# Performance work log

Hardware: AMD Instinct MI355X
Metric: run time of the kernel (lower is better)

Reference implementation:

```python
import jax, jax.numpy as jnp
import numpy as np

N, E, F_IN, D, H, ED = 100000, 250000, 10, 128, 4, 5  # nodes, edges, feat_dim, hidden, heads, edge_dim

def setup_inputs() -> dict:
    key = jax.random.key(0)
    ks = jax.random.split(key, 16)
    def w(k, shape, fan_in):
        return (jax.random.normal(k, shape, jnp.float32) / np.sqrt(fan_in).astype(np.float32))
    return {
        "x": jax.random.normal(ks[0], (N, F_IN), jnp.float32),
        "edge_index": jax.random.randint(ks[1], (2, E), 0, N, dtype=jnp.int32),
        "edge_attr": jax.random.uniform(ks[2], (E, ED), jnp.float32),
        "batch": jnp.zeros((N,), jnp.int32),
        # input_proj: Linear(10,128) + BN
        "W_in": w(ks[3], (F_IN, D), F_IN), "b_in": jnp.zeros((D,), jnp.float32),
        "g_in": jnp.ones((D,), jnp.float32), "beta_in": jnp.zeros((D,), jnp.float32),
        # GINEConv: edge lin (5->128) + MLP 128->256->128 with BN
        "We": w(ks[4], (ED, D), ED), "be": jnp.zeros((D,), jnp.float32),
        "W1": w(ks[5], (D, 2 * D), D), "b1": jnp.zeros((2 * D,), jnp.float32),
        "g1": jnp.ones((2 * D,), jnp.float32), "beta1": jnp.zeros((2 * D,), jnp.float32),
        "W2": w(ks[6], (2 * D, D), 2 * D), "b2": jnp.zeros((D,), jnp.float32),
        # skip weights (pre-sigmoid) and per-layer BatchNorms
        "skip0": jnp.float32(0.5), "skip1": jnp.float32(0.5),
        "g_n0": jnp.ones((D,), jnp.float32), "b_n0": jnp.zeros((D,), jnp.float32),
        "g_n1": jnp.ones((D,), jnp.float32), "b_n1": jnp.zeros((D,), jnp.float32),
        # GATv2Conv(128,128,heads=4,concat=False,edge_dim=5)
        "Wl": w(ks[7], (D, H * D), D), "bl": jnp.zeros((H * D,), jnp.float32),
        "Wr": w(ks[8], (D, H * D), D), "br": jnp.zeros((H * D,), jnp.float32),
        "att": w(ks[9], (H, D), D),
        "W_eg": w(ks[10], (ED, H * D), ED),
        "bias_gat": jnp.zeros((D,), jnp.float32),
    }

def _bn(h, g, b):
    # BatchNorm1d with batch statistics (deterministic), eps=1e-5
    m = h.mean(axis=0)
    v = jnp.var(h, axis=0)
    return (h - m) * jax.lax.rsqrt(v + 1e-5) * g + b

def reference(x, edge_index, edge_attr, batch,
              W_in, b_in, g_in, beta_in,
              We, be, W1, b1, g1, beta1, W2, b2,
              skip0, skip1, g_n0, b_n0, g_n1, b_n1,
              Wl, bl, Wr, br, att, W_eg, bias_gat):
    n = x.shape[0]
    src, dst = edge_index[0], edge_index[1]
    # input projection (dropout off / eval)
    x = jax.nn.relu(_bn(x @ W_in + b_in, g_in, beta_in))
    layer0 = x
    # ---- GINEConv: sum_j relu(x_j + lin(edge_attr)), then MLP on (1+eps)*x + agg, eps=0 ----
    e_proj = edge_attr @ We + be                              # [E, D]
    msg = jax.nn.relu(x[src] + e_proj)                        # [E, D]
    agg = jax.ops.segment_sum(msg, dst, num_segments=n)       # [N, D]
    h = x + agg
    h = jax.nn.relu(_bn(h @ W1 + b1, g1, beta1)) @ W2 + b2
    x_new = jax.nn.relu(h)
    s0 = jax.nn.sigmoid(skip0)
    x = _bn(s0 * x + (1.0 - s0) * x_new, g_n0, b_n0)
    layer1 = x
    # ---- GATv2Conv (heads=4, concat=False -> mean over heads) ----
    xl = (x @ Wl + bl).reshape(n, H, D)                       # source transform
    xr = (x @ Wr + br).reshape(n, H, D)                       # target transform
    eg = (edge_attr @ W_eg).reshape(-1, H, D)                 # edge transform (no bias)
    feat = xl[src] + xr[dst] + eg                             # [E, H, D]
    logits = jnp.einsum('ehd,hd->eh', jax.nn.leaky_relu(feat, 0.2), att)  # [E, H]
    mx = jax.ops.segment_max(logits, dst, num_segments=n)     # segment softmax over in-edges of dst
    ex = jnp.exp(logits - mx[dst])
    den = jax.ops.segment_sum(ex, dst, num_segments=n)
    alpha = ex / den[dst]                                     # [E, H]
    out = jax.ops.segment_sum(alpha[:, :, None] * xl[src], dst, num_segments=n)  # [N, H, D]
    x_new = jax.nn.relu(out.mean(axis=1) + bias_gat)
    s1 = jax.nn.sigmoid(skip1)
    x = _bn(s1 * x + (1.0 - s1) * x_new, g_n1, b_n1)
    final = (layer0 + layer1 + x) / 3.0
    return final
```

## Files before the change

kernel.cpp:

```cpp
#include <hip/hip_runtime.h>
#include <stdint.h>

__device__ __forceinline__ float relu_(float v){ return v > 0.f ? v : 0.f; }

typedef _Float16 f16;
typedef f16 f16x8 __attribute__((ext_vector_type(8)));
typedef float f32x4 __attribute__((ext_vector_type(4)));

__device__ __forceinline__ f16x8 u2h(uint4 u){ union{uint4 u; f16x8 h;} c; c.u=u; return c.h; }

#define STD_BN(p, idx) ((p) + (size_t)(idx) * 4096)

__global__ __launch_bounds__(256) void k_hist(const int* __restrict__ dst,
                                              int* __restrict__ cnt, int E)
{
  int e = blockIdx.x*256 + threadIdx.x;
  if (e < E) atomicAdd(&cnt[dst[e]], 1);
}

__global__ __launch_bounds__(256) void k_scan1(const int* __restrict__ cnt,
    int* __restrict__ off, int* __restrict__ bsum, int N)
{
  __shared__ int part[256];
  int tid = threadIdx.x;
  int base = blockIdx.x*1024 + tid*4;
  int v[4]; int s = 0;
  #pragma unroll
  for (int j = 0; j < 4; ++j) { v[j] = (base + j < N) ? cnt[base + j] : 0; s += v[j]; }
  part[tid] = s;
  __syncthreads();
  #pragma unroll
  for (int d = 1; d < 256; d <<= 1) {
    int tv = (tid >= d) ? part[tid - d] : 0;
    __syncthreads();
    part[tid] += tv;
    __syncthreads();
  }
  int run = part[tid] - s;
  #pragma unroll
  for (int j = 0; j < 4; ++j) {
    run += v[j];
    if (base + j < N) off[base + j + 1] = run;
  }
  if (tid == 255) bsum[blockIdx.x] = part[255];
}

__global__ void k_scan2(const int* __restrict__ bsum, int* __restrict__ bofs, int nb)
{
  if (threadIdx.x == 0) {
    int run = 0;
    for (int b = 0; b < nb; ++b) { bofs[b] = run; run += bsum[b]; }
  }
}

__global__ __launch_bounds__(256) void k_scan3(int* __restrict__ off,
    const int* __restrict__ bofs, int N)
{
  int tid = threadIdx.x;
  int base = blockIdx.x*1024 + tid*4;
  int add = bofs[blockIdx.x];
  #pragma unroll
  for (int j = 0; j < 4; ++j)
    if (base + j < N) off[base + j + 1] += add;
  if (blockIdx.x == 0 && tid == 0) off[0] = 0;
}

__global__ __launch_bounds__(256) void k_fill(const int* __restrict__ dst,
    const int* __restrict__ off, int* __restrict__ fill,
    int* __restrict__ eid, int E)
{
  int e = blockIdx.x*256 + threadIdx.x;
  if (e >= E) return;
  int t = dst[e];
  int pos = off[t] + atomicAdd(&fill[t], 1);
  eid[pos] = e;
}

__global__ __launch_bounds__(64) void k_packB(
  const float* __restrict__ W, int ldw, int cb,
  int ct0, int nks, int nctFull, uint4* __restrict__ Bpk)
{
  int ks  = blockIdx.x % nks;
  int ctl = blockIdx.x / nks;
  int lane = threadIdx.x;
  int col = cb + ctl*16 + (lane & 15);
  int kbase = ks*32 + (lane >> 4)*8;
  f16x8 hi, lo;
  #pragma unroll
  for (int i = 0; i < 8; ++i) {
    float w = W[(size_t)(kbase + i)*ldw + col];
    f16 h = (f16)w;
    hi[i] = h;
    lo[i] = (f16)(w - (float)h);
  }
  union{f16x8 h; uint4 u;} ch, cl; ch.h = hi; cl.h = lo;
  size_t idx = ((size_t)(ks*nctFull + ct0 + ctl)*64 + lane)*2;
  Bpk[idx] = ch.u;
  Bpk[idx + 1] = cl.u;
}

__global__ void k_packbias(const float* __restrict__ bl, const float* __restrict__ br,
                           float* __restrict__ bp)
{
  int c = threadIdx.x, h = blockIdx.x;
  bp[h*256 + c] = (c < 128) ? bl[h*128 + c] : br[h*128 + (c - 128)];
}

template<int PREP, int EPI, int K, int NT>
__global__ __launch_bounds__(256) void k_mfma(
  const float* __restrict__ A0, const float* __restrict__ A1,
  const float* __restrict__ STF, int stfofs,
  const uint4* __restrict__ Bpk, const float* __restrict__ biasp,
  const float* __restrict__ l0, const float* __restrict__ sk,
  float* __restrict__ OUT, int N)
{
  __shared__ float As[64][68];
  constexpr int NCT = NT/16;
  const int tid = threadIdx.x;
  const int lane = tid & 63, wv = tid >> 6;
  const int fr = lane & 15, fg = lane >> 4;
  const int row0 = blockIdx.x * 64;
  f32x4 acc[NCT];
  #pragma unroll
  for (int ct = 0; ct < NCT; ++ct) acc[ct] = (f32x4){0.f, 0.f, 0.f, 0.f};

  const int sr = tid >> 2;
  const int sc = (tid & 3) * 16;
  for (int kb = 0; kb < K; kb += 64) {
    int r = row0 + sr;
    #pragma unroll
    for (int j = 0; j < 4; ++j) {
      int c = sc + j*4;
      int k = kb + c;
      float4 v = make_float4(0.f, 0.f, 0.f, 0.f);
      if (r < N) {
        if (PREP == 0) {
          float4 a = *(const float4*)(A0 + (size_t)r*K + k);
          float4 b = *(const float4*)(A1 + (size_t)r*K + k);
          v.x = a.x+b.x; v.y = a.y+b.y; v.z = a.z+b.z; v.w = a.w+b.w;
        } else {
          float4 a  = *(const float4*)(A0 + (size_t)r*K + k);
          float4 aa = *(const float4*)(STF + stfofs + k);
          float4 cc = *(const float4*)(STF + stfofs + 256 + k);
          v.x = aa.x*a.x + cc.x; v.y = aa.y*a.y + cc.y;
          v.z = aa.z*a.z + cc.z; v.w = aa.w*a.w + cc.w;
          if (PREP == 1) { v.x=relu_(v.x); v.y=relu_(v.y); v.z=relu_(v.z); v.w=relu_(v.w); }
        }
      }
      *(float4*)&As[sr][c] = v;
    }
    __syncthreads();
    #pragma unroll
    for (int k2 = 0; k2 < 2; ++k2) {
      const float* ap = &As[wv*16 + fr][k2*32 + fg*8];
      f16x8 ah, al;
      #pragma unroll
      for (int i = 0; i < 8; ++i) {
        float a = ap[i];
        f16 h = (f16)a;
        ah[i] = h;
        al[i] = (f16)(a - (float)h);
      }
      int ks = (kb >> 5) + k2;
      const uint4* bp = Bpk + ((size_t)ks*NCT*64 + lane)*2;
      #pragma unroll
      for (int ct = 0; ct < NCT; ++ct) {
        f16x8 bh = u2h(bp[ct*128]);
        f16x8 bl = u2h(bp[ct*128 + 1]);
        acc[ct] = __builtin_amdgcn_mfma_f32_16x16x32_f16(ah, bh, acc[ct], 0, 0, 0);
        acc[ct] = __builtin_amdgcn_mfma_f32_16x16x32_f16(ah, bl, acc[ct], 0, 0, 0);
        acc[ct] = __builtin_amdgcn_mfma_f32_16x16x32_f16(al, bh, acc[ct], 0, 0, 0);
      }
    }
    __syncthreads();
  }
  float s0g = 0.f, os0 = 0.f;
  if (EPI == 1) { s0g = 1.f/(1.f + expf(-sk[0])); os0 = 1.f - s0g; }
  #pragma unroll
  for (int ct = 0; ct < NCT; ++ct) {
    int col = ct*16 + fr;
    float bv = biasp[col];
    #pragma unroll
    for (int rr = 0; rr < 4; ++rr) {
      int row = row0 + wv*16 + fg*4 + rr;
      if (row < N) {
        float v = acc[ct][rr] + bv;
        if (EPI == 1) v = s0g*l0[(size_t)row*128 + col] + os0*relu_(v);
        OUT[(size_t)row*NT + col] = v;
      }
    }
  }
}

__global__ __launch_bounds__(256) void k_inproj(
    const float* __restrict__ x, const float* __restrict__ W_in,
    const float* __restrict__ b_in, float* __restrict__ y0,
    double* __restrict__ STD0, int N)
{
  const int d  = threadIdx.x & 127;
  const int ro = threadIdx.x >> 7;
  float w[10];
  #pragma unroll
  for (int k = 0; k < 10; ++k) w[k] = W_in[k*128 + d];
  const float bi = b_in[d];
  int r0 = blockIdx.x * 128;
  int rend = min(r0 + 128, N);
  double sum = 0.0, sqs = 0.0;
  for (int r = r0 + ro; r < rend; r += 2) {
    const float* xr = x + (size_t)r * 10;
    float acc = bi;
    #pragma unroll
    for (int k = 0; k < 10; ++k) acc += xr[k] * w[k];
    y0[(size_t)r*128 + d] = acc;
    double a = (double)acc;
    sum += a; sqs += a*a;
  }
  int slice = ((blockIdx.x & 3) << 1) | ro;
  atomicAdd(&STD0[slice*512 + d], sum);
  atomicAdd(&STD0[slice*512 + 256 + d], sqs);
}

__global__ void k_bnfin(const double* __restrict__ STDbn,
                        const float* __restrict__ g, const float* __restrict__ beta,
                        float* __restrict__ STFbn, int colofs, double invN)
{
  int col = colofs + threadIdx.x;
  double s = 0.0, q = 0.0;
  #pragma unroll
  for (int sl = 0; sl < 8; ++sl) {
    s += STDbn[sl*512 + col];
    q += STDbn[sl*512 + 256 + col];
  }
  double m = s * invN;
  double var = q * invN - m*m;
  double av = (double)g[col] / sqrt(var + 1e-5);
  STFbn[col] = (float)av;
  STFbn[256 + col] = (float)((double)beta[col] - m*av);
}

__global__ __launch_bounds__(256) void k_affrelu(float* __restrict__ buf,
    const float* __restrict__ STF0, long total4)
{
  long g = (long)blockIdx.x*256 + threadIdx.x;
  if (g >= total4) return;
  int d0 = (int)((g*4) & 127);
  float4 v = ((const float4*)buf)[g];
  float4 av = *(const float4*)(STF0 + d0);
  float4 bv = *(const float4*)(STF0 + 256 + d0);
  v.x = relu_(av.x*v.x + bv.x);
  v.y = relu_(av.y*v.y + bv.y);
  v.z = relu_(av.z*v.z + bv.z);
  v.w = relu_(av.w*v.w + bv.w);
  ((float4*)buf)[g] = v;
}

template<int C>
__global__ __launch_bounds__(256) void k_colstats(
  const float* __restrict__ p, double* __restrict__ STDr, int N)
{
  int r0 = blockIdx.x * 64;
  int rend = min(r0 + 64, N);
  double s = 0.0, q = 0.0;
  int col, slice;
  if (C == 128) {
    col = threadIdx.x & 127;
    int ro = threadIdx.x >> 7;
    for (int r = r0 + ro; r < rend; r += 2) {
      double v = (double)p[(size_t)r*C + col];
      s += v; q += v*v;
    }
    slice = ((blockIdx.x & 3) << 1) | ro;
  } else {
    col = threadIdx.x;
    for (int r = r0; r < rend; ++r) {
      double v = (double)p[(size_t)r*C + col];
      s += v; q += v*v;
    }
    slice = blockIdx.x & 7;
  }
  atomicAdd(&STDr[slice*512 + col], s);
  atomicAdd(&STDr[slice*512 + 256 + col], q);
}

__global__ __launch_bounds__(256) void k_gine_gather(
  const int* __restrict__ off, const int* __restrict__ eid,
  const int* __restrict__ src, const float* __restrict__ eattr,
  const float* __restrict__ We, const float* __restrict__ be,
  const float* __restrict__ L0, float* __restrict__ AG, int N)
{
  int wv = threadIdx.x >> 6, lane = threadIdx.x & 63;
  int t = blockIdx.x*4 + wv;
  if (t >= N) return;
  int o0 = off[t], deg = off[t+1] - o0;
  float2 w2[5];
  #pragma unroll
  for (int i = 0; i < 5; ++i) w2[i] = *(const float2*)(We + i*128 + 2*lane);
  float2 be2 = *(const float2*)(be + 2*lane);
  float2 acc = make_float2(0.f, 0.f);
  for (int base = 0; base < deg; base += 64) {
    int cn = min(64, deg - base);
    int sL = 0; float eaL[5] = {0,0,0,0,0};
    if (lane < cn) {
      int eL = eid[o0 + base + lane];
      sL = src[eL];
      #pragma unroll
      for (int j = 0; j < 5; ++j) eaL[j] = eattr[(size_t)eL*5 + j];
    }
    for (int i = 0; i < cn; ++i) {
      int s_i = __shfl(sL, i);
      float2 xl2 = *(const float2*)(L0 + (size_t)s_i*128 + 2*lane);
      float ex = be2.x, ey = be2.y;
      #pragma unroll
      for (int j = 0; j < 5; ++j) {
        float ea = __shfl(eaL[j], i);
        ex += ea*w2[j].x; ey += ea*w2[j].y;
      }
      acc.x += relu_(xl2.x + ex);
      acc.y += relu_(xl2.y + ey);
    }
  }
  *((float2*)(AG + (size_t)t*128) + lane) = acc;
}

#define GCAP 12

#define GAT_EDGE(IDX, POUT, XLOUT) { \
  int e_ = eid[o0 + (IDX)]; int s_ = src[e_]; \
  XLOUT = *(const float2*)(X2 + (size_t)s_*256 + 2*lane); \
  const float* ep_ = eattr + (size_t)e_*5; \
  float fx_ = XLOUT.x + xr2.x, fy_ = XLOUT.y + xr2.y; \
  _Pragma("unroll") \
  for (int j5_ = 0; j5_ < 5; ++j5_) { float ea_ = ep_[j5_]; fx_ += ea_*w2[j5_].x; fy_ += ea_*w2[j5_].y; } \
  fx_ = fx_ > 0.f ? fx_ : 0.2f*fx_; \
  fy_ = fy_ > 0.f ? fy_ : 0.2f*fy_; \
  float pp_ = fx_*at2.x + fy_*at2.y; \
  _Pragma("unroll") \
  for (int mm_ = 1; mm_ < 64; mm_ <<= 1) pp_ += __shfl_xor(pp_, mm_, 64); \
  POUT = pp_; }

__global__ __launch_bounds__(256) void k_gat_attn(
  const int* __restrict__ off, const int* __restrict__ eid,
  const int* __restrict__ src, const float* __restrict__ eattr,
  const float* __restrict__ X2, const float* __restrict__ Weg,
  const float* __restrict__ att, float* __restrict__ AG,
  int N, int h, int first)
{
  int wv = threadIdx.x >> 6, lane = threadIdx.x & 63;
  int t = blockIdx.x*4 + wv;
  if (t >= N) return;
  int o0 = off[t], deg = off[t+1] - o0;
  float2* AGrow = (float2*)(AG + (size_t)t*128) + lane;
  if (deg == 0) { if (first) *AGrow = make_float2(0.f, 0.f); return; }
  int dcol = h*128 + 2*lane;
  float2 xr2 = *(const float2*)(X2 + (size_t)t*256 + 128 + 2*lane);
  float2 at2 = *(const float2*)(att + dcol);
  float2 w2[5];
  #pragma unroll
  for (int i = 0; i < 5; ++i) w2[i] = *(const float2*)(Weg + i*512 + dcol);

  if (deg <= GCAP) {
    int sL = 0; float eaL[5] = {0,0,0,0,0};
    if (lane < deg) {
      int eL = eid[o0 + lane];
      sL = src[eL];
      #pragma unroll
      for (int j = 0; j < 5; ++j) eaL[j] = eattr[(size_t)eL*5 + j];
    }
    float lg[GCAP]; float2 xb[GCAP];
    float mx = -1e30f;
    #pragma unroll
    for (int i = 0; i < GCAP; ++i) {
      if (i < deg) {
        int s_i = __shfl(sL, i);
        float2 xl2 = *(const float2*)(X2 + (size_t)s_i*256 + 2*lane);
        float fx = xl2.x + xr2.x, fy = xl2.y + xr2.y;
        #pragma unroll
        for (int j = 0; j < 5; ++j) {
          float ea = __shfl(eaL[j], i);
          fx += ea*w2[j].x; fy += ea*w2[j].y;
        }
        fx = fx > 0.f ? fx : 0.2f*fx;
        fy = fy > 0.f ? fy : 0.2f*fy;
        float p = fx*at2.x + fy*at2.y;
        #pragma unroll
        for (int m = 1; m < 64; m <<= 1) p += __shfl_xor(p, m, 64);
        lg[i] = p; xb[i] = xl2;
        mx = fmaxf(mx, p);
      }
    }
    float den = 0.f;
    #pragma unroll
    for (int i = 0; i < GCAP; ++i)
      if (i < deg) { lg[i] = expf(lg[i] - mx); den += lg[i]; }
    float sc = 0.25f / den;
    float2 acc = make_float2(0.f, 0.f);
    #pragma unroll
    for (int i = 0; i < GCAP; ++i)
      if (i < deg) { acc.x += lg[i]*xb[i].x; acc.y += lg[i]*xb[i].y; }
    float2 prev = first ? make_float2(0.f,0.f) : *AGrow;
    *AGrow = make_float2(prev.x + sc*acc.x, prev.y + sc*acc.y);
  } else {
    float mx = -1e30f;
    for (int i = 0; i < deg; ++i) { float p; float2 xl2; GAT_EDGE(i, p, xl2); mx = fmaxf(mx, p); (void)xl2; }
    float den = 0.f;
    for (int i = 0; i < deg; ++i) { float p; float2 xl2; GAT_EDGE(i, p, xl2); den += expf(p - mx); (void)xl2; }
    float sc = 0.25f / den;
    float2 acc = make_float2(0.f, 0.f);
    for (int i = 0; i < deg; ++i) {
      float p; float2 xl2; GAT_EDGE(i, p, xl2);
      float al = expf(p - mx);
      acc.x += al*xl2.x; acc.y += al*xl2.y;
    }
    float2 prev = first ? make_float2(0.f,0.f) : *AGrow;
    *AGrow = make_float2(prev.x + sc*acc.x, prev.y + sc*acc.y);
  }
}

__global__ __launch_bounds__(128) void k_gat_post(
  float* __restrict__ AG, const float* __restrict__ P1,
  const float* __restrict__ STF, const float* __restrict__ bias_gat,
  const float* __restrict__ skip1, double* __restrict__ STD3, int N)
{
  int d = threadIdx.x;
  float an0 = STF[1024 + d], bn0 = STF[1280 + d];
  float bg = bias_gat[d];
  float s1g = 1.f/(1.f + expf(-skip1[0]));
  float os1 = 1.f - s1g;
  int r0 = blockIdx.x * 256;
  int rend = min(r0 + 256, N);
  double sum = 0.0, sqs = 0.0;
  for (int r = r0; r < rend; ++r) {
    size_t idx = (size_t)r*128 + d;
    float xn = relu_(AG[idx] + bg);
    float l1 = an0*P1[idx] + bn0;
    float p2 = s1g*l1 + os1*xn;
    AG[idx] = p2;
    double dv = (double)p2;
    sum += dv; sqs += dv*dv;
  }
  int slice = blockIdx.x & 7;
  atomicAdd(&STD3[slice*512 + d], sum);
  atomicAdd(&STD3[slice*512 + 256 + d], sqs);
}

__global__ __launch_bounds__(256) void k_final(
  float* __restrict__ L0, const float* __restrict__ P1,
  const float* __restrict__ pre2, const float* __restrict__ STF, long total4)
{
  long g = (long)blockIdx.x*256 + threadIdx.x;
  if (g >= total4) return;
  int d0 = (int)((g*4) & 127);
  float4 a0 = *(const float4*)(STF + 1024 + d0);
  float4 b0 = *(const float4*)(STF + 1280 + d0);
  float4 a1 = *(const float4*)(STF + 1536 + d0);
  float4 b1 = *(const float4*)(STF + 1792 + d0);
  float4 v0 = ((const float4*)L0)[g];
  float4 v1 = ((const float4*)P1)[g];
  float4 v2 = ((const float4*)pre2)[g];
  float4 o;
  const float k3 = 1.f/3.f;
  o.x = (v0.x + (a0.x*v1.x + b0.x) + (a1.x*v2.x + b1.x)) * k3;
  o.y = (v0.y + (a0.y*v1.y + b0.y) + (a1.y*v2.y + b1.y)) * k3;
  o.z = (v0.z + (a0.z*v1.z + b0.z) + (a1.z*v2.z + b1.z)) * k3;
  o.w = (v0.w + (a0.w*v1.w + b0.w) + (a1.w*v2.w + b1.w)) * k3;
  ((float4*)L0)[g] = o;
}

extern "C" void kernel_launch(void* const* d_in, const int* in_sizes, int n_in,
                              void* d_out, int out_size, void* d_ws, size_t ws_size,
                              hipStream_t stream)
{
  const float* x       = (const float*)d_in[0];
  const int*   eidx    = (const int*)  d_in[1];
  const float* eattr   = (const float*)d_in[2];
  const float* W_in    = (const float*)d_in[4];
  const float* b_in    = (const float*)d_in[5];
  const float* g_in    = (const float*)d_in[6];
  const float* beta_in = (const float*)d_in[7];
  const float* We      = (const float*)d_in[8];
  const float* be      = (const float*)d_in[9];
  const float* W1      = (const float*)d_in[10];
  const float* b1      = (const float*)d_in[11];
  const float* g1      = (const float*)d_in[12];
  const float* beta1   = (const float*)d_in[13];
  const float* W2      = (const float*)d_in[14];
  const float* b2      = (const float*)d_in[15];
  const float* skip0   = (const float*)d_in[16];
  const float* skip1   = (const float*)d_in[17];
  const float* g_n0    = (const float*)d_in[18];
  const float* b_n0    = (const float*)d_in[19];
  const float* g_n1    = (const float*)d_in[20];
  const float* b_n1    = (const float*)d_in[21];
  const float* Wl      = (const float*)d_in[22];
  const float* bl      = (const float*)d_in[23];
  const float* Wr      = (const float*)d_in[24];
  const float* br      = (const float*)d_in[25];
  const float* att     = (const float*)d_in[26];
  const float* Weg     = (const float*)d_in[27];
  const float* bias_g  = (const float*)d_in[28];

  const int N = in_sizes[0] / 10;
  const int E = in_sizes[1] / 2;
  const int* srcv = eidx;
  const int* dstv = eidx + E;

  float* L0 = (float*)d_out;

  char* wsb = (char*)d_ws;
  const size_t szN128 = (size_t)N*128*4;
  size_t oSTD = 0;
  size_t oSTF = oSTD + 131072;
  size_t oAG  = oSTF + 8192;
  size_t oP1  = oAG + szN128;
  size_t oX2  = oP1 + szN128;
  size_t oCNT = oX2 + 2*szN128;
  size_t oFIL = oCNT + (size_t)N*4;
  size_t oOFF = oFIL + (size_t)N*4;
  size_t oEID = oOFF + (size_t)(N+1)*4;
  size_t oBS  = oEID + (size_t)E*4;
  size_t oBOF = oBS + 1024;
  size_t oBP1 = oBOF + 1024;
  size_t oBP2 = oBP1 + 8192*16;
  size_t oBPG = oBP2 + 8192*16;
  size_t oBPB = oBPG + 4*8192*16;

  double* STD = (double*)(wsb + oSTD);
  float*  STF = (float*) (wsb + oSTF);
  float*  AG  = (float*) (wsb + oAG);
  float*  P1  = (float*) (wsb + oP1);
  float*  X2  = (float*) (wsb + oX2);
  int*    CNT = (int*)   (wsb + oCNT);
  int*    FIL = (int*)   (wsb + oFIL);
  int*    OFF = (int*)   (wsb + oOFF);
  int*    EID = (int*)   (wsb + oEID);
  int*    BS  = (int*)   (wsb + oBS);
  int*    BOF = (int*)   (wsb + oBOF);
  uint4*  BP1 = (uint4*) (wsb + oBP1);
  uint4*  BP2 = (uint4*) (wsb + oBP2);
  uint4*  BPG = (uint4*) (wsb + oBPG);
  float*  BPB = (float*) (wsb + oBPB);

  const double invN = 1.0 / (double)N;
  const int nb = (N + 63)/64;
  const int nscan = (N + 1023)/1024;

  hipMemsetAsync(STD, 0, 131072, stream);
  hipMemsetAsync(CNT, 0, (size_t)N*4, stream);
  hipMemsetAsync(FIL, 0, (size_t)N*4, stream);

  k_packB<<<16*4, 64, 0, stream>>>(W1, 256, 0, 0, 4, 16, BP1);
  k_packB<<<8*8,  64, 0, stream>>>(W2, 128, 0, 0, 8, 8,  BP2);
  for (int h = 0; h < 4; ++h) {
    k_packB<<<8*4, 64, 0, stream>>>(Wl, 512, h*128, 0, 4, 16, BPG + (size_t)h*8192);
    k_packB<<<8*4, 64, 0, stream>>>(Wr, 512, h*128, 8, 4, 16, BPG + (size_t)h*8192);
  }
  k_packbias<<<4, 256, 0, stream>>>(bl, br, BPB);

  k_hist <<<(E + 255)/256, 256, 0, stream>>>(dstv, CNT, E);
  k_scan1<<<nscan, 256, 0, stream>>>(CNT, OFF, BS, N);
  k_scan2<<<1, 64, 0, stream>>>(BS, BOF, nscan);
  k_scan3<<<nscan, 256, 0, stream>>>(OFF, BOF, N);
  k_fill <<<(E + 255)/256, 256, 0, stream>>>(dstv, OFF, FIL, EID, E);

  k_inproj<<<(N + 127)/128, 256, 0, stream>>>(x, W_in, b_in, L0, STD_BN(STD,0), N);
  k_bnfin<<<1, 128, 0, stream>>>(STD_BN(STD,0), g_in, beta_in, STF + 0, 0, invN);
  {
    long t4 = (long)N*32;
    k_affrelu<<<(unsigned)((t4 + 255)/256), 256, 0, stream>>>(L0, STF + 0, t4);
  }

  k_gine_gather<<<(N + 3)/4, 256, 0, stream>>>(OFF, EID, srcv, eattr, We, be, L0, AG, N);

  k_mfma<0,0,128,256><<<nb, 256, 0, stream>>>(L0, AG, STF, 0, BP1, b1, nullptr, nullptr, X2, N);
  k_colstats<256><<<nb, 256, 0, stream>>>(X2, STD_BN(STD,1), N);
  k_bnfin<<<1, 256, 0, stream>>>(STD_BN(STD,1), g1, beta1, STF + 512, 0, invN);
  k_mfma<1,1,256,128><<<nb, 256, 0, stream>>>(X2, nullptr, STF, 512, BP2, b2, L0, skip0, P1, N);
  k_colstats<128><<<nb, 256, 0, stream>>>(P1, STD_BN(STD,2), N);
  k_bnfin<<<1, 128, 0, stream>>>(STD_BN(STD,2), g_n0, b_n0, STF + 1024, 0, invN);

  for (int h = 0; h < 4; ++h) {
    k_mfma<2,0,128,256><<<nb, 256, 0, stream>>>(P1, nullptr, STF, 1024,
                                                BPG + (size_t)h*8192, BPB + h*256,
                                                nullptr, nullptr, X2, N);
    k_gat_attn<<<(N + 3)/4, 256, 0, stream>>>(OFF, EID, srcv, eattr, X2, Weg, att,
                                              AG, N, h, (h == 0) ? 1 : 0);
  }

  k_gat_post<<<(N + 255)/256, 128, 0, stream>>>(AG, P1, STF, bias_g, skip1, STD_BN(STD,3), N);
  k_bnfin<<<1, 128, 0, stream>>>(STD_BN(STD,3), g_n1, b_n1, STF + 1536, 0, invN);
  {
    long t4 = (long)N*32;
    k_final<<<(unsigned)((t4 + 255)/256), 256, 0, stream>>>(L0, P1, AG, STF, t4);
  }
  (void)n_in; (void)out_size; (void)ws_size;
}
```

Baseline: 1.260 ms.

## Load MFMA A-fragments directly from global with register prefetch, drop LDS staging

Each lane now loads its own A fragment (8 contiguous floats of its row) straight from global memory into registers, and prefetches the next k-slice while the current one feeds the MFMAs. This removes the shared-memory tile and the two block-wide barriers per k-block. In exchange the global loads are less coalesced (strided per row across lanes), the STF scale/shift vectors are reloaded per lane, and register pressure rises from the fully unrolled K loop.

```diff
diff --git a/kernel.cpp b/kernel.cpp
--- a/kernel.cpp
+++ b/kernel.cpp
@@ -114,66 +114,73 @@
   const float* __restrict__ l0, const float* __restrict__ sk,
   float* __restrict__ OUT, int N)
 {
-  __shared__ float As[64][68];
   constexpr int NCT = NT/16;
+  constexpr int KS = K/32;
   const int tid = threadIdx.x;
   const int lane = tid & 63, wv = tid >> 6;
   const int fr = lane & 15, fg = lane >> 4;
   const int row0 = blockIdx.x * 64;
+  const int arowi = row0 + wv*16 + fr;
+  const bool avalid = arowi < N;
+  const float* arow  = A0 + (size_t)(avalid ? arowi : 0) * K;
+  const float* arow1 = (PREP == 0) ? (A1 + (size_t)(avalid ? arowi : 0) * K) : (const float*)nullptr;
+
   f32x4 acc[NCT];
   #pragma unroll
   for (int ct = 0; ct < NCT; ++ct) acc[ct] = (f32x4){0.f, 0.f, 0.f, 0.f};
 
-  const int sr = tid >> 2;
-  const int sc = (tid & 3) * 16;
-  for (int kb = 0; kb < K; kb += 64) {
-    int r = row0 + sr;
+  auto loadA = [&](int ks, float4& va, float4& vb) {
+    int k = ks*32 + fg*8;
+    float4 x = *(const float4*)(arow + k);
+    float4 y = *(const float4*)(arow + k + 4);
+    if (PREP == 0) {
+      float4 g0 = *(const float4*)(arow1 + k);
+      float4 g1 = *(const float4*)(arow1 + k + 4);
+      x.x += g0.x; x.y += g0.y; x.z += g0.z; x.w += g0.w;
+      y.x += g1.x; y.y += g1.y; y.z += g1.z; y.w += g1.w;
+    } else {
+      float4 a0 = *(const float4*)(STF + stfofs + k);
+      float4 a1 = *(const float4*)(STF + stfofs + k + 4);
+      float4 c0 = *(const float4*)(STF + stfofs + 256 + k);
+      float4 c1 = *(const float4*)(STF + stfofs + 256 + k + 4);
+      x.x = a0.x*x.x + c0.x; x.y = a0.y*x.y + c0.y;
+      x.z = a0.z*x.z + c0.z; x.w = a0.w*x.w + c0.w;
+      y.x = a1.x*y.x + c1.x; y.y = a1.y*y.y + c1.y;
+      y.z = a1.z*y.z + c1.z; y.w = a1.w*y.w + c1.w;
+      if (PREP == 1) {
+        x.x = relu_(x.x); x.y = relu_(x.y); x.z = relu_(x.z); x.w = relu_(x.w);
+        y.x = relu_(y.x); y.y = relu_(y.y); y.z = relu_(y.z); y.w = relu_(y.w);
+      }
+    }
+    if (!avalid) { x = make_float4(0,0,0,0); y = make_float4(0,0,0,0); }
+    va = x; vb = y;
+  };
+
+  float4 cva, cvb, nva, nvb;
+  loadA(0, cva, cvb);
+  #pragma unroll
+  for (int ks = 0; ks < KS; ++ks) {
+    if (ks + 1 < KS) loadA(ks + 1, nva, nvb);
+    float av[8] = {cva.x,cva.y,cva.z,cva.w,cvb.x,cvb.y,cvb.z,cvb.w};
+    f16x8 ah, al;
     #pragma unroll
-    for (int j = 0; j < 4; ++j) {
-      int c = sc + j*4;
-      int k = kb + c;
-      float4 v = make_float4(0.f, 0.f, 0.f, 0.f);
-      if (r < N) {
-        if (PREP == 0) {
-          float4 a = *(const float4*)(A0 + (size_t)r*K + k);
-          float4 b = *(const float4*)(A1 + (size_t)r*K + k);
-          v.x = a.x+b.x; v.y = a.y+b.y; v.z = a.z+b.z; v.w = a.w+b.w;
-        } else {
-          float4 a  = *(const float4*)(A0 + (size_t)r*K + k);
-          float4 aa = *(const float4*)(STF + stfofs + k);
-          float4 cc = *(const float4*)(STF + stfofs + 256 + k);
-          v.x = aa.x*a.x + cc.x; v.y = aa.y*a.y + cc.y;
-          v.z = aa.z*a.z + cc.z; v.w = aa.w*a.w + cc.w;
-          if (PREP == 1) { v.x=relu_(v.x); v.y=relu_(v.y); v.z=relu_(v.z); v.w=relu_(v.w); }
-        }
-      }
-      *(float4*)&As[sr][c] = v;
-    }
-    __syncthreads();
+    for (int i = 0; i < 8; ++i) {
+      f16 h = (f16)av[i];
+      ah[i] = h;
+      al[i] = (f16)(av[i] - (float)h);
+    }
+    const uint4* bp = Bpk + ((size_t)ks*NCT*64 + lane)*2;
     #pragma unroll
-    for (int k2 = 0; k2 < 2; ++k2) {
-      const float* ap = &As[wv*16 + fr][k2*32 + fg*8];
-      f16x8 ah, al;
-      #pragma unroll
-      for (int i = 0; i < 8; ++i) {
-        float a = ap[i];
-        f16 h = (f16)a;
-        ah[i] = h;
-        al[i] = (f16)(a - (float)h);
-      }
-      int ks = (kb >> 5) + k2;
-      const uint4* bp = Bpk + ((size_t)ks*NCT*64 + lane)*2;
-      #pragma unroll
-      for (int ct = 0; ct < NCT; ++ct) {
-        f16x8 bh = u2h(bp[ct*128]);
-        f16x8 bl = u2h(bp[ct*128 + 1]);
-        acc[ct] = __builtin_amdgcn_mfma_f32_16x16x32_f16(ah, bh, acc[ct], 0, 0, 0);
-        acc[ct] = __builtin_amdgcn_mfma_f32_16x16x32_f16(ah, bl, acc[ct], 0, 0, 0);
-        acc[ct] = __builtin_amdgcn_mfma_f32_16x16x32_f16(al, bh, acc[ct], 0, 0, 0);
-      }
-    }
-    __syncthreads();
-  }
+    for (int ct = 0; ct < NCT; ++ct) {
+      f16x8 bh = u2h(bp[ct*128]);
+      f16x8 bl = u2h(bp[ct*128 + 1]);
+      acc[ct] = __builtin_amdgcn_mfma_f32_16x16x32_f16(ah, bh, acc[ct], 0, 0, 0);
+      acc[ct] = __builtin_amdgcn_mfma_f32_16x16x32_f16(ah, bl, acc[ct], 0, 0, 0);
+      acc[ct] = __builtin_amdgcn_mfma_f32_16x16x32_f16(al, bh, acc[ct], 0, 0, 0);
+    }
+    cva = nva; cvb = nvb;
+  }
+
   float s0g = 0.f, os0 = 0.f;
   if (EPI == 1) { s0g = 1.f/(1.f + expf(-sk[0])); os0 = 1.f - s0g; }
   #pragma unroll
```

After: 1.194 ms. 5.2% less time.
